# Performance work log

Hardware: AMD Instinct MI355X
Metric: run time of the kernel (lower is better)

Reference implementation:

```python
import jax, jax.numpy as jnp
import numpy as np
import math

D_MODEL = 1024
NUM_HEADS = 16
D_FF = 4096
LN_EPS = 1e-5


def _layer_norm(x, gamma, beta):
    mu = jnp.mean(x, axis=-1, keepdims=True)
    var = jnp.mean(jnp.square(x - mu), axis=-1, keepdims=True)
    return (x - mu) / jnp.sqrt(var + LN_EPS) * gamma + beta


def setup_inputs() -> dict:
    key = jax.random.key(0)
    ks = jax.random.split(key, 16)
    S, B, D, F = 2048, 2, D_MODEL, D_FF
    sc = 0.02
    inp = {
        "x": jax.random.normal(ks[0], (S, B, D), dtype=jnp.float32),
        "Wq": jax.random.normal(ks[1], (D, D), dtype=jnp.float32) * sc,
        "bq": jnp.zeros((D,), jnp.float32),
        "Wk": jax.random.normal(ks[2], (D, D), dtype=jnp.float32) * sc,
        "bk": jnp.zeros((D,), jnp.float32),
        "Wv": jax.random.normal(ks[3], (D, D), dtype=jnp.float32) * sc,
        "bv": jnp.zeros((D,), jnp.float32),
        "Wo": jax.random.normal(ks[4], (D, D), dtype=jnp.float32) * sc,
        "bo": jnp.zeros((D,), jnp.float32),
        "g1": jnp.ones((D,), jnp.float32),
        "b1": jnp.zeros((D,), jnp.float32),
        "W1": jax.random.normal(ks[5], (D, F), dtype=jnp.float32) * sc,
        "bb1": jnp.zeros((F,), jnp.float32),
        "W2": jax.random.normal(ks[6], (F, D), dtype=jnp.float32) * sc,
        "bb2": jnp.zeros((D,), jnp.float32),
        "g2": jnp.ones((D,), jnp.float32),
        "b2": jnp.zeros((D,), jnp.float32),
    }
    return inp


def reference(x, Wq, bq, Wk, bk, Wv, bv, Wo, bo, g1, b1, W1, bb1, W2, bb2, g2, b2):
    # x: [S, B, D] (seq-first, matching the torch module)
    S, B, D = x.shape
    H = NUM_HEADS
    dh = D // H

    def split_(t):  # [S, B, D] -> [B*H, S, dh]  (same as view + transpose in torch)
        return jnp.swapaxes(t.reshape(S, B * H, dh), 0, 1)

    q = split_(x @ Wq + bq)
    k = split_(x @ Wk + bk)
    v = split_(x @ Wv + bv)

    # naive bmm -> softmax -> bmm attention (full [B*H, S, S] scores)
    scores = jnp.einsum("nsd,ntd->nst", q / math.sqrt(dh), k)
    attn = jax.nn.softmax(scores, axis=-1)
    o = jnp.einsum("nst,ntd->nsd", attn, v)  # [B*H, S, dh]
    o = jnp.swapaxes(o, 0, 1).reshape(S, B, D) @ Wo + bo

    x1 = _layer_norm(x + o, g1, b1)
    ff = jax.nn.relu(x1 @ W1 + bb1) @ W2 + bb2
    return _layer_norm(x1 + ff, g2, b2)
```

## Files before the change

### kernel.cpp

```cpp
#include <hip/hip_runtime.h>
#include <hip/hip_bf16.h>
#include <cstdint>

typedef __bf16 bf16_t;
typedef __attribute__((ext_vector_type(8))) __bf16 bf16x8;
typedef __attribute__((ext_vector_type(4))) __bf16 bf16x4;
typedef __attribute__((ext_vector_type(2))) __bf16 bf16x2;
typedef __attribute__((ext_vector_type(4))) float f32x4;

#define GLOBAL_AS __attribute__((address_space(1)))
#define LDS_AS __attribute__((address_space(3)))

__device__ __forceinline__ void lds_load16(void* lds, const void* g) {
    __builtin_amdgcn_global_load_lds((GLOBAL_AS void*)g, (LDS_AS void*)lds, 16, 0, 0);
}

__global__ __launch_bounds__(256) void cast_f32_bf16(const float* __restrict__ in,
                                                     bf16_t* __restrict__ out, int n4) {
    int i = (blockIdx.x * 256 + threadIdx.x);
    if (i >= n4) return;
    float4 v = *(const float4*)(in + (size_t)i * 4);
    bf16x4 o;
    o[0] = (bf16_t)v.x; o[1] = (bf16_t)v.y; o[2] = (bf16_t)v.z; o[3] = (bf16_t)v.w;
    *(bf16x4*)(out + (size_t)i * 4) = o;
}

__global__ __launch_bounds__(256) void transpose_cast(const float* __restrict__ W,
                                                      bf16_t* __restrict__ WT,
                                                      int Kd, int Nd) {
    __shared__ float T[64][65];
    const int nbk = Kd >> 6;
    const int bk = blockIdx.x % nbk, bn = blockIdx.x / nbk;
    const int k0 = bk << 6, n0 = bn << 6;
    const int tid = threadIdx.x;
    #pragma unroll
    for (int rep = 0; rep < 4; ++rep) {
        int r = rep * 16 + (tid >> 4);
        int c = (tid & 15) * 4;
        float4 v = *(const float4*)(W + (size_t)(k0 + r) * Nd + n0 + c);
        T[r][c] = v.x; T[r][c + 1] = v.y; T[r][c + 2] = v.z; T[r][c + 3] = v.w;
    }
    __syncthreads();
    #pragma unroll
    for (int rep = 0; rep < 4; ++rep) {
        int r = rep * 16 + (tid >> 4);
        int c = (tid & 15) * 4;
        bf16x4 o;
        o[0] = (bf16_t)T[c][r]; o[1] = (bf16_t)T[c + 1][r];
        o[2] = (bf16_t)T[c + 2][r]; o[3] = (bf16_t)T[c + 3][r];
        *(bf16x4*)(WT + (size_t)(n0 + r) * Kd + k0 + c) = o;
    }
}

__global__ __launch_bounds__(256) void concat_bias(const float* a, const float* b,
                                                   const float* c, float* o) {
    int i = blockIdx.x * 256 + threadIdx.x;
    o[i] = (i < 1024) ? a[i] : (i < 2048) ? b[i - 1024] : c[i - 2048];
}

template <int OM, bool RELU>
__global__ __launch_bounds__(512, 2) void gemm256(const bf16_t* __restrict__ A,
                                                  const bf16_t* __restrict__ Bt,
                                                  const float* __restrict__ bias,
                                                  void* __restrict__ Cv,
                                                  int M, int N, int K,
                                                  int kc_len, int n_kc) {
    __shared__ alignas(16) bf16_t As[2][256 * 64];
    __shared__ alignas(16) bf16_t Bs[2][256 * 64];
    const int tid = threadIdx.x;
    const int wid = tid >> 6, lane = tid & 63;
    const int lr = lane & 15, lg = lane >> 4;
    const int wr = wid >> 2, wc = wid & 3;
    const int lrsw = (lr & 7) << 4;

    const int nbn = N >> 8;
    const int nbase = (M >> 8) * nbn;
    const int nwg = nbase * n_kc;
    int bid = blockIdx.x;
    int wg;
    if ((nwg & 7) == 0) { int q = nwg >> 3; wg = (bid & 7) * q + (bid >> 3); }
    else wg = bid;
    const int kc = wg / nbase;
    const int inner = wg - kc * nbase;
    const int bm = inner / nbn, bn = inner % nbn;

    f32x4 acc[8][4];
    #pragma unroll
    for (int i = 0; i < 8; ++i)
        #pragma unroll
        for (int j = 0; j < 4; ++j) acc[i][j] = f32x4{0.f, 0.f, 0.f, 0.f};

    const int srow = wid * 16 + (lane >> 3);
    const int colbyte = (((lane & 7) ^ (lane >> 3)) << 4);
    const char* gA = (const char*)(A + ((size_t)(bm * 256 + srow) * K + kc * kc_len)) + colbyte;
    const char* gB = (const char*)(Bt + ((size_t)(bn * 256 + srow) * K + kc * kc_len)) + colbyte;
    const size_t rs8 = (size_t)8 * K * 2;
    const size_t rs128 = (size_t)128 * K * 2;

    auto stA = [&](int b, int half, int kt) {
        char* d = (char*)As[b] + (half * 128 + wid * 16) * 128;
        const char* s = gA + (size_t)half * rs128 + (size_t)kt * 128;
        lds_load16(d, s);
        lds_load16(d + 1024, s + rs8);
    };
    auto stB = [&](int b, int half, int kt) {
        char* d = (char*)Bs[b] + (half * 128 + wid * 16) * 128;
        const char* s = gB + (size_t)half * rs128 + (size_t)kt * 128;
        lds_load16(d, s);
        lds_load16(d + 1024, s + rs8);
    };
    auto ldA = [&](int b, int m, int kk) {
        const int row = (m >> 2) * 128 + (m & 3) * 32 + wr * 16 + lr;
        return *(const bf16x8*)((const char*)As[b] + row * 128 + ((kk * 64 + lg * 16) ^ lrsw));
    };
    auto ldB = [&](int b, int n, int kk) {
        const int row = n * 64 + wc * 16 + lr;
        return *(const bf16x8*)((const char*)Bs[b] + row * 128 + ((kk * 64 + lg * 16) ^ lrsw));
    };

    const int NT = kc_len >> 6;
    stA(0, 0, 0); stB(0, 0, 0); stB(0, 1, 0); stA(0, 1, 0);
    asm volatile("s_waitcnt vmcnt(4)" ::: "memory");
    __builtin_amdgcn_s_barrier();

    bf16x8 afr[4][2], bfr[4][2];
    #pragma unroll 1
    for (int kt = 0; kt < NT; ++kt) {
        const int buf = kt & 1;
        const int ktn = (kt + 1 < NT) ? kt + 1 : kt;

        #pragma unroll
        for (int m = 0; m < 4; ++m) {
            afr[m][0] = ldA(buf, m, 0);
            afr[m][1] = ldA(buf, m, 1);
        }
        #pragma unroll
        for (int n = 0; n < 2; ++n) {
            bfr[n][0] = ldB(buf, n, 0);
            bfr[n][1] = ldB(buf, n, 1);
        }
        stA(buf ^ 1, 0, ktn);
        __builtin_amdgcn_s_barrier();
        __builtin_amdgcn_s_setprio(1);
        #pragma unroll
        for (int m = 0; m < 4; ++m)
            #pragma unroll
            for (int n = 0; n < 2; ++n) {
                acc[m][n] = __builtin_amdgcn_mfma_f32_16x16x32_bf16(afr[m][0], bfr[n][0], acc[m][n], 0, 0, 0);
                acc[m][n] = __builtin_amdgcn_mfma_f32_16x16x32_bf16(afr[m][1], bfr[n][1], acc[m][n], 0, 0, 0);
            }
        __builtin_amdgcn_s_setprio(0);
        asm volatile("s_waitcnt vmcnt(4)" ::: "memory");
        __builtin_amdgcn_s_barrier();

        #pragma unroll
        for (int n = 2; n < 4; ++n) {
            bfr[n][0] = ldB(buf, n, 0);
            bfr[n][1] = ldB(buf, n, 1);
        }
        stB(buf ^ 1, 0, ktn);
        __builtin_amdgcn_s_barrier();
        __builtin_amdgcn_s_setprio(1);
        #pragma unroll
        for (int m = 0; m < 4; ++m)
            #pragma unroll
            for (int n = 2; n < 4; ++n) {
                acc[m][n] = __builtin_amdgcn_mfma_f32_16x16x32_bf16(afr[m][0], bfr[n][0], acc[m][n], 0, 0, 0);
                acc[m][n] = __builtin_amdgcn_mfma_f32_16x16x32_bf16(afr[m][1], bfr[n][1], acc[m][n], 0, 0, 0);
            }
        __builtin_amdgcn_s_setprio(0);
        asm volatile("s_waitcnt vmcnt(4)" ::: "memory");
        __builtin_amdgcn_s_barrier();

        #pragma unroll
        for (int m = 0; m < 4; ++m) {
            afr[m][0] = ldA(buf, m + 4, 0);
            afr[m][1] = ldA(buf, m + 4, 1);
        }
        stB(buf ^ 1, 1, ktn);
        __builtin_amdgcn_s_barrier();
        __builtin_amdgcn_s_setprio(1);
        #pragma unroll
        for (int m = 0; m < 4; ++m)
            #pragma unroll
            for (int n = 0; n < 2; ++n) {
                acc[m + 4][n] = __builtin_amdgcn_mfma_f32_16x16x32_bf16(afr[m][0], bfr[n][0], acc[m + 4][n], 0, 0, 0);
                acc[m + 4][n] = __builtin_amdgcn_mfma_f32_16x16x32_bf16(afr[m][1], bfr[n][1], acc[m + 4][n], 0, 0, 0);
            }
        __builtin_amdgcn_s_setprio(0);
        __builtin_amdgcn_s_barrier();

        stA(buf ^ 1, 1, ktn);
        __builtin_amdgcn_s_barrier();
        __builtin_amdgcn_s_setprio(1);
        #pragma unroll
        for (int m = 0; m < 4; ++m)
            #pragma unroll
            for (int n = 2; n < 4; ++n) {
                acc[m + 4][n] = __builtin_amdgcn_mfma_f32_16x16x32_bf16(afr[m][0], bfr[n][0], acc[m + 4][n], 0, 0, 0);
                acc[m + 4][n] = __builtin_amdgcn_mfma_f32_16x16x32_bf16(afr[m][1], bfr[n][1], acc[m + 4][n], 0, 0, 0);
            }
        __builtin_amdgcn_s_setprio(0);
        asm volatile("s_waitcnt vmcnt(4)" ::: "memory");
        __builtin_amdgcn_s_barrier();
    }

    float* outf = (float*)Cv + (size_t)kc * M * N;
    bf16_t* outb = (bf16_t*)Cv + (size_t)kc * M * N;
    float bv[4];
    #pragma unroll
    for (int n = 0; n < 4; ++n) {
        const int c = (bn << 8) + n * 64 + wc * 16 + lr;
        bv[n] = (bias && kc == 0) ? bias[c] : 0.f;
    }
    #pragma unroll
    for (int m = 0; m < 8; ++m) {
        const int row0 = (bm << 8) + (m >> 2) * 128 + (m & 3) * 32 + wr * 16 + (lg << 2);
        #pragma unroll
        for (int n = 0; n < 4; ++n) {
            const int c = (bn << 8) + n * 64 + wc * 16 + lr;
            #pragma unroll
            for (int j = 0; j < 4; ++j) {
                float v = acc[m][n][j] + bv[n];
                if (RELU) v = fmaxf(v, 0.f);
                if (OM == 0)      ((bf16_t*)Cv)[(size_t)(row0 + j) * N + c] = (bf16_t)v;
                else if (OM == 1) outf[(size_t)(row0 + j) * N + c] = v;
                else              outb[(size_t)(row0 + j) * N + c] = (bf16_t)v;
            }
        }
    }
}

__global__ __launch_bounds__(256) void reshape_qkv(const bf16_t* __restrict__ QKV,
                                                   bf16_t* __restrict__ Q,
                                                   bf16_t* __restrict__ Kh,
                                                   bf16_t* __restrict__ VT) {
    __shared__ alignas(16) bf16_t Vl[64][72];
    const int n = blockIdx.x >> 5, st = blockIdx.x & 31;
    const int b = n >> 4, h = n & 15;
    const int s0 = st << 6;
    const int tid = threadIdx.x;
    const float qscale = 0.125f * 1.4426950408889634f;

    #pragma unroll
    for (int mat = 0; mat < 2; ++mat) {
        bf16_t* dst = mat ? Kh : Q;
        #pragma unroll
        for (int rep = 0; rep < 2; ++rep) {
            int chunk = rep * 256 + tid;
            int sl = chunk >> 3, c8 = (chunk & 7) << 3;
            size_t srow = (size_t)(s0 + sl) * 2 + b;
            bf16x8 v = *(const bf16x8*)(QKV + srow * 3072 + mat * 1024 + h * 64 + c8);
            if (mat == 0) {
                #pragma unroll
                for (int e = 0; e < 8; ++e) v[e] = (bf16_t)((float)v[e] * qscale);
            }
            *(bf16x8*)(dst + ((size_t)n * 2048 + s0 + sl) * 64 + c8) = v;
        }
    }
    #pragma unroll
    for (int rep = 0; rep < 2; ++rep) {
        int chunk = rep * 256 + tid;
        int sl = chunk >> 3, c8 = (chunk & 7) << 3;
        size_t srow = (size_t)(s0 + sl) * 2 + b;
        *(bf16x8*)&Vl[sl][c8] = *(const bf16x8*)(QKV + srow * 3072 + 2048 + h * 64 + c8);
    }
    __syncthreads();
    #pragma unroll
    for (int rep = 0; rep < 2; ++rep) {
        int chunk = rep * 256 + tid;
        int d = chunk >> 3, c8 = (chunk & 7) << 3;
        bf16x8 v;
        #pragma unroll
        for (int e = 0; e < 8; ++e) v[e] = Vl[c8 + e][d];
        *(bf16x8*)(VT + ((size_t)n * 64 + d) * 2048 + s0 + c8) = v;
    }
}

__global__ __launch_bounds__(256) void attn_fwd(const bf16_t* __restrict__ Q,
                                                const bf16_t* __restrict__ K,
                                                const bf16_t* __restrict__ VT,
                                                bf16_t* __restrict__ O) {
    const int S = 2048;
    const int n = blockIdx.x >> 4;
    const int qt = blockIdx.x & 15;
    const int q0 = qt << 7;
    const int tid = threadIdx.x, wid = tid >> 6, lane = tid & 63;
    const int lr = lane & 15, lg = lane >> 4;
    const int lrsw = (lr & 7) << 4;

    __shared__ alignas(16) bf16_t Ks[2][64 * 64];
    __shared__ alignas(16) bf16_t Vs[2][64 * 64];
    __shared__ alignas(16) bf16_t Ps[4][2][16 * 64];

    char* pbs0 = (char*)&Ps[wid][0][0];
    char* pbs1 = (char*)&Ps[wid][1][0];

    const bf16_t* Qrow0 = Q + ((size_t)n * S + q0 + wid * 32 + lr) * 64;
    const bf16_t* Qrow1 = Qrow0 + 16 * 64;
    const bf16x8 qa0 = *(const bf16x8*)(Qrow0 + lg * 8);
    const bf16x8 qa1 = *(const bf16x8*)(Qrow0 + 32 + lg * 8);
    const bf16x8 qb0 = *(const bf16x8*)(Qrow1 + lg * 8);
    const bf16x8 qb1 = *(const bf16x8*)(Qrow1 + 32 + lg * 8);

    bf16x8 ones;
    #pragma unroll
    for (int e = 0; e < 8; ++e) ones[e] = (bf16_t)1.0f;

    const int colbyte = (((lane & 7) ^ (lane >> 3)) << 4);
    const char* ksrc0 = (const char*)(K + ((size_t)n * S + wid * 16 + (lane >> 3)) * 64) + colbyte;
    const char* ksrc1 = ksrc0 + (size_t)8 * 128;
    const char* vsrc0 = (const char*)(VT + ((size_t)n * 64 + wid * 16 + (lane >> 3)) * S) + colbyte;
    const char* vsrc1 = vsrc0 + (size_t)8 * S * 2;

    auto stage = [&](int b, int t0) {
        lds_load16((char*)Ks[b] + wid * 2048,        ksrc0 + (size_t)t0 * 128);
        lds_load16((char*)Ks[b] + wid * 2048 + 1024, ksrc1 + (size_t)t0 * 128);
        lds_load16((char*)Vs[b] + wid * 2048,        vsrc0 + (size_t)t0 * 2);
        lds_load16((char*)Vs[b] + wid * 2048 + 1024, vsrc1 + (size_t)t0 * 2);
    };

    f32x4 oaccA[4], oaccB[4];
    #pragma unroll
    for (int i = 0; i < 4; ++i) {
        oaccA[i] = f32x4{0.f, 0.f, 0.f, 0.f};
        oaccB[i] = f32x4{0.f, 0.f, 0.f, 0.f};
    }
    f32x4 laccA = f32x4{0.f, 0.f, 0.f, 0.f};
    f32x4 laccB = f32x4{0.f, 0.f, 0.f, 0.f};

    stage(0, 0);
    int buf = 0;

    #pragma unroll 1
    for (int t0 = 0; t0 < S; t0 += 64) {
        if (t0 + 64 < S) {
            stage(buf ^ 1, t0 + 64);
            asm volatile("s_waitcnt vmcnt(4)" ::: "memory");
        } else {
            asm volatile("s_waitcnt vmcnt(0)" ::: "memory");
        }
        __builtin_amdgcn_s_barrier();

        const char* kb = (char*)Ks[buf];
        const char* vb = (char*)Vs[buf];

        f32x4 swA[4], swB[4];
        #pragma unroll
        for (int tc = 0; tc < 4; ++tc) {
            const char* krow = kb + (tc * 16 + lr) * 128;
            bf16x8 kf0 = *(const bf16x8*)(krow + ((lg * 16) ^ lrsw));
            bf16x8 kf1 = *(const bf16x8*)(krow + ((64 + lg * 16) ^ lrsw));
            f32x4 za = f32x4{-12.f, -12.f, -12.f, -12.f};
            za = __builtin_amdgcn_mfma_f32_16x16x32_bf16(kf0, qa0, za, 0, 0, 0);
            za = __builtin_amdgcn_mfma_f32_16x16x32_bf16(kf1, qa1, za, 0, 0, 0);
            swA[tc] = za;
            f32x4 zb = f32x4{-12.f, -12.f, -12.f, -12.f};
            zb = __builtin_amdgcn_mfma_f32_16x16x32_bf16(kf0, qb0, zb, 0, 0, 0);
            zb = __builtin_amdgcn_mfma_f32_16x16x32_bf16(kf1, qb1, zb, 0, 0, 0);
            swB[tc] = zb;
        }

        #pragma unroll
        for (int tc = 0; tc < 4; ++tc)
            #pragma unroll
            for (int j = 0; j < 4; ++j) {
                swA[tc][j] = __builtin_amdgcn_exp2f(swA[tc][j]);
                swB[tc][j] = __builtin_amdgcn_exp2f(swB[tc][j]);
            }

        #pragma unroll
        for (int tc = 0; tc < 4; ++tc)
            #pragma unroll
            for (int hh = 0; hh < 2; ++hh) {
                bf16x2 pa, pb;
                pa[0] = (bf16_t)swA[tc][2 * hh]; pa[1] = (bf16_t)swA[tc][2 * hh + 1];
                pb[0] = (bf16_t)swB[tc][2 * hh]; pb[1] = (bf16_t)swB[tc][2 * hh + 1];
                const int off = (tc * 32 + lg * 8 + hh * 4) ^ lrsw;
                *(bf16x2*)(pbs0 + lr * 128 + off) = pa;
                *(bf16x2*)(pbs1 + lr * 128 + off) = pb;
            }
        bf16x8 pA0 = *(const bf16x8*)(pbs0 + lr * 128 + ((lg * 16) ^ lrsw));
        bf16x8 pA1 = *(const bf16x8*)(pbs0 + lr * 128 + ((64 + lg * 16) ^ lrsw));
        bf16x8 pB0 = *(const bf16x8*)(pbs1 + lr * 128 + ((lg * 16) ^ lrsw));
        bf16x8 pB1 = *(const bf16x8*)(pbs1 + lr * 128 + ((64 + lg * 16) ^ lrsw));

        laccA = __builtin_amdgcn_mfma_f32_16x16x32_bf16(ones, pA0, laccA, 0, 0, 0);
        laccA = __builtin_amdgcn_mfma_f32_16x16x32_bf16(ones, pA1, laccA, 0, 0, 0);
        laccB = __builtin_amdgcn_mfma_f32_16x16x32_bf16(ones, pB0, laccB, 0, 0, 0);
        laccB = __builtin_amdgcn_mfma_f32_16x16x32_bf16(ones, pB1, laccB, 0, 0, 0);

        #pragma unroll
        for (int vc = 0; vc < 4; ++vc) {
            const char* vrow = vb + (vc * 16 + lr) * 128;
            bf16x8 vf0 = *(const bf16x8*)(vrow + ((lg * 16) ^ lrsw));
            bf16x8 vf1 = *(const bf16x8*)(vrow + ((64 + lg * 16) ^ lrsw));
            oaccA[vc] = __builtin_amdgcn_mfma_f32_16x16x32_bf16(vf0, pA0, oaccA[vc], 0, 0, 0);
            oaccA[vc] = __builtin_amdgcn_mfma_f32_16x16x32_bf16(vf1, pA1, oaccA[vc], 0, 0, 0);
            oaccB[vc] = __builtin_amdgcn_mfma_f32_16x16x32_bf16(vf0, pB0, oaccB[vc], 0, 0, 0);
            oaccB[vc] = __builtin_amdgcn_mfma_f32_16x16x32_bf16(vf1, pB1, oaccB[vc], 0, 0, 0);
        }
        __builtin_amdgcn_s_barrier();
        buf ^= 1;
    }

    const int b = n >> 4, h = n & 15;
    const float invA = 1.0f / laccA[0];
    const float invB = 1.0f / laccB[0];
    const size_t tokA = (size_t)(q0 + wid * 32 + lr) * 2 + b;
    const size_t tokB = tokA + 32;
    #pragma unroll
    for (int vc = 0; vc < 4; ++vc) {
        bf16x4 oa, ob;
        #pragma unroll
        for (int j = 0; j < 4; ++j) {
            oa[j] = (bf16_t)(oaccA[vc][j] * invA);
            ob[j] = (bf16_t)(oaccB[vc][j] * invB);
        }
        *(bf16x4*)(O + tokA * 1024 + h * 64 + vc * 16 + lg * 4) = oa;
        *(bf16x4*)(O + tokB * 1024 + h * 64 + vc * 16 + lg * 4) = ob;
    }
}

template <int P>
__global__ __launch_bounds__(256) void ln_res(const float* __restrict__ X,
                                              const bf16_t* __restrict__ Y,
                                              const float* __restrict__ g,
                                              const float* __restrict__ be,
                                              float* __restrict__ outf,
                                              bf16_t* __restrict__ outb) {
    const int row = blockIdx.x, tid = threadIdx.x;
    const size_t base = (size_t)row * 1024 + tid * 4;
    const size_t pstride = (size_t)4096 * 1024;
    float4 xv = *(const float4*)(X + base);
    float v0 = xv.x, v1 = xv.y, v2 = xv.z, v3 = xv.w;
    #pragma unroll
    for (int p = 0; p < P; ++p) {
        bf16x4 yv = *(const bf16x4*)(Y + p * pstride + base);
        v0 += (float)yv[0]; v1 += (float)yv[1]; v2 += (float)yv[2]; v3 += (float)yv[3];
    }
    float s = v0 + v1 + v2 + v3;
    float sq = v0 * v0 + v1 * v1 + v2 * v2 + v3 * v3;
    #pragma unroll
    for (int m = 1; m < 64; m <<= 1) {
        s += __shfl_xor(s, m);
        sq += __shfl_xor(sq, m);
    }
    __shared__ float rs[4], rq[4];
    const int wid = tid >> 6;
    if ((tid & 63) == 0) { rs[wid] = s; rq[wid] = sq; }
    __syncthreads();
    s = rs[0] + rs[1] + rs[2] + rs[3];
    sq = rq[0] + rq[1] + rq[2] + rq[3];
    const float mu = s * (1.f / 1024.f);
    const float var = sq * (1.f / 1024.f) - mu * mu;
    const float rstd = rsqrtf(var + 1e-5f);
    float4 gv = *(const float4*)(g + tid * 4);
    float4 bv = *(const float4*)(be + tid * 4);
    float o0 = (v0 - mu) * rstd * gv.x + bv.x;
    float o1 = (v1 - mu) * rstd * gv.y + bv.y;
    float o2 = (v2 - mu) * rstd * gv.z + bv.z;
    float o3 = (v3 - mu) * rstd * gv.w + bv.w;
    float4 ov = {o0, o1, o2, o3};
    *(float4*)(outf + base) = ov;
    if (outb) {
        bf16x4 ob;
        ob[0] = (bf16_t)o0; ob[1] = (bf16_t)o1; ob[2] = (bf16_t)o2; ob[3] = (bf16_t)o3;
        *(bf16x4*)(outb + base) = ob;
    }
}

extern "C" void kernel_launch(void* const* d_in, const int* in_sizes, int n_in,
                              void* d_out, int out_size, void* d_ws, size_t ws_size,
                              hipStream_t stream) {
    (void)in_sizes; (void)n_in; (void)out_size; (void)ws_size;
    const float* x   = (const float*)d_in[0];
    const float* Wq  = (const float*)d_in[1];
    const float* bq  = (const float*)d_in[2];
    const float* Wk  = (const float*)d_in[3];
    const float* bk  = (const float*)d_in[4];
    const float* Wv  = (const float*)d_in[5];
    const float* bv  = (const float*)d_in[6];
    const float* Wo  = (const float*)d_in[7];
    const float* bo  = (const float*)d_in[8];
    const float* g1  = (const float*)d_in[9];
    const float* b1  = (const float*)d_in[10];
    const float* W1  = (const float*)d_in[11];
    const float* bb1 = (const float*)d_in[12];
    const float* W2  = (const float*)d_in[13];
    const float* bb2 = (const float*)d_in[14];
    const float* g2  = (const float*)d_in[15];
    const float* b2  = (const float*)d_in[16];
    float* out = (float*)d_out;

    char* ws = (char*)d_ws;
    const size_t MB = 1ull << 20;
    bf16_t* xb    = (bf16_t*)(ws + 0);
    bf16_t* WqkvT = (bf16_t*)(ws + 8 * MB);
    bf16_t* WoT   = (bf16_t*)(ws + 14 * MB);
    bf16_t* W1T   = (bf16_t*)(ws + 16 * MB);
    bf16_t* W2T   = (bf16_t*)(ws + 24 * MB);
    float*  qkvb  = (float*)(ws + 32 * MB);
    bf16_t* QKV   = (bf16_t*)(ws + 33 * MB);
    bf16_t* WoP   = (bf16_t*)(ws + 33 * MB);
    bf16_t* W2P   = (bf16_t*)(ws + 33 * MB);
    bf16_t* Qh    = (bf16_t*)(ws + 65 * MB);
    bf16_t* Kh    = (bf16_t*)(ws + 73 * MB);
    bf16_t* VTh   = (bf16_t*)(ws + 81 * MB);
    float*  x1f   = (float*)(ws + 97 * MB);
    bf16_t* x1b   = (bf16_t*)(ws + 113 * MB);
    bf16_t* Hff   = (bf16_t*)(ws + 121 * MB);
    bf16_t* Otok  = (bf16_t*)(ws + 153 * MB);

    cast_f32_bf16<<<4096, 256, 0, stream>>>(x, xb, 1024 * 1024);
    transpose_cast<<<256, 256, 0, stream>>>(Wq, WqkvT, 1024, 1024);
    transpose_cast<<<256, 256, 0, stream>>>(Wk, WqkvT + 1024 * 1024, 1024, 1024);
    transpose_cast<<<256, 256, 0, stream>>>(Wv, WqkvT + 2048 * 1024, 1024, 1024);
    transpose_cast<<<256, 256, 0, stream>>>(Wo, WoT, 1024, 1024);
    transpose_cast<<<1024, 256, 0, stream>>>(W1, W1T, 1024, 4096);
    transpose_cast<<<1024, 256, 0, stream>>>(W2, W2T, 4096, 1024);
    concat_bias<<<12, 256, 0, stream>>>(bq, bk, bv, qkvb);

    gemm256<0, false><<<192, 512, 0, stream>>>(xb, WqkvT, qkvb, QKV, 4096, 3072, 1024, 1024, 1);
    reshape_qkv<<<1024, 256, 0, stream>>>(QKV, Qh, Kh, VTh);
    attn_fwd<<<512, 256, 0, stream>>>(Qh, Kh, VTh, Otok);
    gemm256<2, false><<<256, 512, 0, stream>>>(Otok, WoT, bo, WoP, 4096, 1024, 1024, 256, 4);
    ln_res<4><<<4096, 256, 0, stream>>>(x, WoP, g1, b1, x1f, x1b);

    gemm256<0, true><<<256, 512, 0, stream>>>(x1b, W1T, bb1, Hff, 4096, 4096, 1024, 1024, 1);
    gemm256<2, false><<<256, 512, 0, stream>>>(Hff, W2T, bb2, W2P, 4096, 1024, 4096, 1024, 4);
    ln_res<4><<<4096, 256, 0, stream>>>(x1f, W2P, g2, b2, out, nullptr);
}
```

Baseline: 248.1 us.

## Load V tiles directly into registers instead of staging through LDS

The attention kernel stops staging V through shared memory. Each wave now loads its V fragments straight from global memory into registers with inline-asm dwordx4 loads. The next tile's loads are double-buffered in two register arrays, with manual vmcnt waits that separate the K LDS loads from the V register loads. This removes V LDS traffic and its share of the LDS budget, at the cost of each of the four waves re-reading the same V data from global/L2 and of higher register pressure. The hand-counted vmcnt values and inline asm outputs the compiler does not know are asynchronous are a correctness and scheduling risk.

```diff
diff --git a/kernel.cpp b/kernel.cpp
--- a/kernel.cpp
+++ b/kernel.cpp
@@ -13,6 +13,12 @@
 
 __device__ __forceinline__ void lds_load16(void* lds, const void* g) {
     __builtin_amdgcn_global_load_lds((GLOBAL_AS void*)g, (LDS_AS void*)lds, 16, 0, 0);
+}
+
+__device__ __forceinline__ bf16x8 vload16(const void* p) {
+    bf16x8 r;
+    asm volatile("global_load_dwordx4 %0, %1, off" : "=&v"(r) : "v"(p));
+    return r;
 }
 
 __global__ __launch_bounds__(256) void cast_f32_bf16(const float* __restrict__ in,
@@ -290,7 +296,6 @@
     const int lrsw = (lr & 7) << 4;
 
     __shared__ alignas(16) bf16_t Ks[2][64 * 64];
-    __shared__ alignas(16) bf16_t Vs[2][64 * 64];
     __shared__ alignas(16) bf16_t Ps[4][2][16 * 64];
 
     char* pbs0 = (char*)&Ps[wid][0][0];
@@ -310,15 +315,7 @@
     const int colbyte = (((lane & 7) ^ (lane >> 3)) << 4);
     const char* ksrc0 = (const char*)(K + ((size_t)n * S + wid * 16 + (lane >> 3)) * 64) + colbyte;
     const char* ksrc1 = ksrc0 + (size_t)8 * 128;
-    const char* vsrc0 = (const char*)(VT + ((size_t)n * 64 + wid * 16 + (lane >> 3)) * S) + colbyte;
-    const char* vsrc1 = vsrc0 + (size_t)8 * S * 2;
-
-    auto stage = [&](int b, int t0) {
-        lds_load16((char*)Ks[b] + wid * 2048,        ksrc0 + (size_t)t0 * 128);
-        lds_load16((char*)Ks[b] + wid * 2048 + 1024, ksrc1 + (size_t)t0 * 128);
-        lds_load16((char*)Vs[b] + wid * 2048,        vsrc0 + (size_t)t0 * 2);
-        lds_load16((char*)Vs[b] + wid * 2048 + 1024, vsrc1 + (size_t)t0 * 2);
-    };
+    const char* vbase = (const char*)VT + ((size_t)(n * 64 + lr) * S + lg * 8) * 2;
 
     f32x4 oaccA[4], oaccB[4];
     #pragma unroll
@@ -329,22 +326,33 @@
     f32x4 laccA = f32x4{0.f, 0.f, 0.f, 0.f};
     f32x4 laccB = f32x4{0.f, 0.f, 0.f, 0.f};
 
-    stage(0, 0);
-    int buf = 0;
-
-    #pragma unroll 1
-    for (int t0 = 0; t0 < S; t0 += 64) {
-        if (t0 + 64 < S) {
-            stage(buf ^ 1, t0 + 64);
-            asm volatile("s_waitcnt vmcnt(4)" ::: "memory");
-        } else {
-            asm volatile("s_waitcnt vmcnt(0)" ::: "memory");
-        }
-        __builtin_amdgcn_s_barrier();
-
-        const char* kb = (char*)Ks[buf];
-        const char* vb = (char*)Vs[buf];
-
+    bf16x8 vA[8], vB[8];
+
+    lds_load16((char*)Ks[0] + wid * 2048,        ksrc0);
+    lds_load16((char*)Ks[0] + wid * 2048 + 1024, ksrc1);
+    #pragma unroll
+    for (int vc = 0; vc < 4; ++vc) {
+        const char* p = vbase + (size_t)vc * (16 * 2048 * 2);
+        vA[2 * vc]     = vload16(p);
+        vA[2 * vc + 1] = vload16(p + 64);
+    }
+    asm volatile("s_waitcnt vmcnt(0)" ::: "memory");
+    __builtin_amdgcn_s_barrier();
+
+    auto tile = [&](int bufK, bf16x8 (&vcur)[8], bf16x8 (&vnext)[8], int t0) {
+        const int t0n = (t0 + 64 < S) ? t0 + 64 : t0;
+        lds_load16((char*)Ks[bufK ^ 1] + wid * 2048,        ksrc0 + (size_t)t0n * 128);
+        lds_load16((char*)Ks[bufK ^ 1] + wid * 2048 + 1024, ksrc1 + (size_t)t0n * 128);
+        #pragma unroll
+        for (int vc = 0; vc < 4; ++vc) {
+            const char* p = vbase + (size_t)vc * (16 * 2048 * 2) + (size_t)t0n * 2;
+            vnext[2 * vc]     = vload16(p);
+            vnext[2 * vc + 1] = vload16(p + 64);
+        }
+        asm volatile("s_waitcnt vmcnt(18)" ::: "memory");
+        __builtin_amdgcn_s_barrier();
+
+        const char* kb = (const char*)Ks[bufK];
         f32x4 swA[4], swB[4];
         #pragma unroll
         for (int tc = 0; tc < 4; ++tc) {
@@ -390,19 +398,23 @@
         laccB = __builtin_amdgcn_mfma_f32_16x16x32_bf16(ones, pB0, laccB, 0, 0, 0);
         laccB = __builtin_amdgcn_mfma_f32_16x16x32_bf16(ones, pB1, laccB, 0, 0, 0);
 
+        asm volatile("s_waitcnt vmcnt(10)" ::: "memory");
         #pragma unroll
         for (int vc = 0; vc < 4; ++vc) {
-            const char* vrow = vb + (vc * 16 + lr) * 128;
-            bf16x8 vf0 = *(const bf16x8*)(vrow + ((lg * 16) ^ lrsw));
-            bf16x8 vf1 = *(const bf16x8*)(vrow + ((64 + lg * 16) ^ lrsw));
-            oaccA[vc] = __builtin_amdgcn_mfma_f32_16x16x32_bf16(vf0, pA0, oaccA[vc], 0, 0, 0);
-            oaccA[vc] = __builtin_amdgcn_mfma_f32_16x16x32_bf16(vf1, pA1, oaccA[vc], 0, 0, 0);
-            oaccB[vc] = __builtin_amdgcn_mfma_f32_16x16x32_bf16(vf0, pB0, oaccB[vc], 0, 0, 0);
-            oaccB[vc] = __builtin_amdgcn_mfma_f32_16x16x32_bf16(vf1, pB1, oaccB[vc], 0, 0, 0);
-        }
-        __builtin_amdgcn_s_barrier();
-        buf ^= 1;
-    }
+            oaccA[vc] = __builtin_amdgcn_mfma_f32_16x16x32_bf16(vcur[2 * vc],     pA0, oaccA[vc], 0, 0, 0);
+            oaccA[vc] = __builtin_amdgcn_mfma_f32_16x16x32_bf16(vcur[2 * vc + 1], pA1, oaccA[vc], 0, 0, 0);
+            oaccB[vc] = __builtin_amdgcn_mfma_f32_16x16x32_bf16(vcur[2 * vc],     pB0, oaccB[vc], 0, 0, 0);
+            oaccB[vc] = __builtin_amdgcn_mfma_f32_16x16x32_bf16(vcur[2 * vc + 1], pB1, oaccB[vc], 0, 0, 0);
+        }
+        __builtin_amdgcn_s_barrier();
+    };
+
+    #pragma unroll 1
+    for (int i = 0; i < 32; i += 2) {
+        tile(0, vA, vB, i * 64);
+        tile(1, vB, vA, i * 64 + 64);
+    }
+    asm volatile("s_waitcnt vmcnt(0)" ::: "memory");
 
     const int b = n >> 4, h = n & 15;
     const float invA = 1.0f / laccA[0];
```

Result: slower. 265.6 us (+7.1%).

## Merge prep kernels into one launch and read Q/K directly from QKV

Applied to the files above, without the earlier changes.

Fuses the x cast, six weight transpose-casts and bias concat into a single prep_all launch, cutting seven kernel launches. The reshape kernel now only transposes V, and attention reads Q (scaled on load) and K directly from the token-major QKV buffer, avoiding writing and re-reading separate head-major Q/K copies. K tile loads now use a larger row stride, which may reduce load coalescing in attention. Workspace buffers are relaid out to match.

```diff
diff --git a/kernel.cpp b/kernel.cpp
--- a/kernel.cpp
+++ b/kernel.cpp
@@ -15,47 +15,65 @@
     __builtin_amdgcn_global_load_lds((GLOBAL_AS void*)g, (LDS_AS void*)lds, 16, 0, 0);
 }
 
-__global__ __launch_bounds__(256) void cast_f32_bf16(const float* __restrict__ in,
-                                                     bf16_t* __restrict__ out, int n4) {
-    int i = (blockIdx.x * 256 + threadIdx.x);
-    if (i >= n4) return;
-    float4 v = *(const float4*)(in + (size_t)i * 4);
-    bf16x4 o;
-    o[0] = (bf16_t)v.x; o[1] = (bf16_t)v.y; o[2] = (bf16_t)v.z; o[3] = (bf16_t)v.w;
-    *(bf16x4*)(out + (size_t)i * 4) = o;
-}
-
-__global__ __launch_bounds__(256) void transpose_cast(const float* __restrict__ W,
-                                                      bf16_t* __restrict__ WT,
-                                                      int Kd, int Nd) {
+__global__ __launch_bounds__(256) void prep_all(const float* __restrict__ x,
+                                                const float* __restrict__ Wq,
+                                                const float* __restrict__ Wk,
+                                                const float* __restrict__ Wv,
+                                                const float* __restrict__ Wo,
+                                                const float* __restrict__ W1,
+                                                const float* __restrict__ W2,
+                                                const float* __restrict__ bq,
+                                                const float* __restrict__ bk,
+                                                const float* __restrict__ bv,
+                                                bf16_t* __restrict__ xb,
+                                                bf16_t* __restrict__ WqkvT,
+                                                bf16_t* __restrict__ WoT,
+                                                bf16_t* __restrict__ W1T,
+                                                bf16_t* __restrict__ W2T,
+                                                float* __restrict__ qkvb) {
     __shared__ float T[64][65];
-    const int nbk = Kd >> 6;
-    const int bk = blockIdx.x % nbk, bn = blockIdx.x / nbk;
-    const int k0 = bk << 6, n0 = bn << 6;
-    const int tid = threadIdx.x;
-    #pragma unroll
-    for (int rep = 0; rep < 4; ++rep) {
-        int r = rep * 16 + (tid >> 4);
-        int c = (tid & 15) * 4;
-        float4 v = *(const float4*)(W + (size_t)(k0 + r) * Nd + n0 + c);
-        T[r][c] = v.x; T[r][c + 1] = v.y; T[r][c + 2] = v.z; T[r][c + 3] = v.w;
-    }
-    __syncthreads();
-    #pragma unroll
-    for (int rep = 0; rep < 4; ++rep) {
-        int r = rep * 16 + (tid >> 4);
-        int c = (tid & 15) * 4;
+    const int bid = blockIdx.x, tid = threadIdx.x;
+    if (bid < 3072) {
+        const float* W; bf16_t* WT; int Kd, Nd, lb;
+        if (bid < 1024) {
+            Kd = 1024; Nd = 1024; lb = bid & 255;
+            const int w = bid >> 8;
+            W  = (w == 0) ? Wq : (w == 1) ? Wk : (w == 2) ? Wv : Wo;
+            WT = (w == 0) ? WqkvT : (w == 1) ? WqkvT + 1048576
+               : (w == 2) ? WqkvT + 2097152 : WoT;
+        } else if (bid < 2048) { W = W1; WT = W1T; Kd = 1024; Nd = 4096; lb = bid - 1024; }
+        else                   { W = W2; WT = W2T; Kd = 4096; Nd = 1024; lb = bid - 2048; }
+        const int nbk = Kd >> 6;
+        const int bk = lb % nbk, bn = lb / nbk;
+        const int k0 = bk << 6, n0 = bn << 6;
+        #pragma unroll
+        for (int rep = 0; rep < 4; ++rep) {
+            int r = rep * 16 + (tid >> 4);
+            int c = (tid & 15) * 4;
+            float4 v = *(const float4*)(W + (size_t)(k0 + r) * Nd + n0 + c);
+            T[r][c] = v.x; T[r][c + 1] = v.y; T[r][c + 2] = v.z; T[r][c + 3] = v.w;
+        }
+        __syncthreads();
+        #pragma unroll
+        for (int rep = 0; rep < 4; ++rep) {
+            int r = rep * 16 + (tid >> 4);
+            int c = (tid & 15) * 4;
+            bf16x4 o;
+            o[0] = (bf16_t)T[c][r]; o[1] = (bf16_t)T[c + 1][r];
+            o[2] = (bf16_t)T[c + 2][r]; o[3] = (bf16_t)T[c + 3][r];
+            *(bf16x4*)(WT + (size_t)(n0 + r) * Kd + k0 + c) = o;
+        }
+    } else if (bid < 7168) {
+        const int i = (bid - 3072) * 256 + tid;
+        float4 v = *(const float4*)(x + (size_t)i * 4);
         bf16x4 o;
-        o[0] = (bf16_t)T[c][r]; o[1] = (bf16_t)T[c + 1][r];
-        o[2] = (bf16_t)T[c + 2][r]; o[3] = (bf16_t)T[c + 3][r];
-        *(bf16x4*)(WT + (size_t)(n0 + r) * Kd + k0 + c) = o;
-    }
-}
-
-__global__ __launch_bounds__(256) void concat_bias(const float* a, const float* b,
-                                                   const float* c, float* o) {
-    int i = blockIdx.x * 256 + threadIdx.x;
-    o[i] = (i < 1024) ? a[i] : (i < 2048) ? b[i - 1024] : c[i - 2048];
+        o[0] = (bf16_t)v.x; o[1] = (bf16_t)v.y; o[2] = (bf16_t)v.z; o[3] = (bf16_t)v.w;
+        *(bf16x4*)(xb + (size_t)i * 4) = o;
+    } else {
+        const int i = (bid - 7168) * 256 + tid;
+        if (i < 3072)
+            qkvb[i] = (i < 1024) ? bq[i] : (i < 2048) ? bk[i - 1024] : bv[i - 2048];
+    }
 }
 
 template <int OM, bool RELU>
@@ -231,33 +249,14 @@
     }
 }
 
-__global__ __launch_bounds__(256) void reshape_qkv(const bf16_t* __restrict__ QKV,
-                                                   bf16_t* __restrict__ Q,
-                                                   bf16_t* __restrict__ Kh,
-                                                   bf16_t* __restrict__ VT) {
+__global__ __launch_bounds__(256) void reshape_v(const bf16_t* __restrict__ QKV,
+                                                 bf16_t* __restrict__ VT) {
     __shared__ alignas(16) bf16_t Vl[64][72];
     const int n = blockIdx.x >> 5, st = blockIdx.x & 31;
     const int b = n >> 4, h = n & 15;
     const int s0 = st << 6;
     const int tid = threadIdx.x;
-    const float qscale = 0.125f * 1.4426950408889634f;
-
-    #pragma unroll
-    for (int mat = 0; mat < 2; ++mat) {
-        bf16_t* dst = mat ? Kh : Q;
-        #pragma unroll
-        for (int rep = 0; rep < 2; ++rep) {
-            int chunk = rep * 256 + tid;
-            int sl = chunk >> 3, c8 = (chunk & 7) << 3;
-            size_t srow = (size_t)(s0 + sl) * 2 + b;
-            bf16x8 v = *(const bf16x8*)(QKV + srow * 3072 + mat * 1024 + h * 64 + c8);
-            if (mat == 0) {
-                #pragma unroll
-                for (int e = 0; e < 8; ++e) v[e] = (bf16_t)((float)v[e] * qscale);
-            }
-            *(bf16x8*)(dst + ((size_t)n * 2048 + s0 + sl) * 64 + c8) = v;
-        }
-    }
+
     #pragma unroll
     for (int rep = 0; rep < 2; ++rep) {
         int chunk = rep * 256 + tid;
@@ -277,14 +276,14 @@
     }
 }
 
-__global__ __launch_bounds__(256) void attn_fwd(const bf16_t* __restrict__ Q,
-                                                const bf16_t* __restrict__ K,
+__global__ __launch_bounds__(256) void attn_fwd(const bf16_t* __restrict__ QKV,
                                                 const bf16_t* __restrict__ VT,
                                                 bf16_t* __restrict__ O) {
     const int S = 2048;
     const int n = blockIdx.x >> 4;
     const int qt = blockIdx.x & 15;
     const int q0 = qt << 7;
+    const int b = n >> 4, h = n & 15;
     const int tid = threadIdx.x, wid = tid >> 6, lane = tid & 63;
     const int lr = lane & 15, lg = lane >> 4;
     const int lrsw = (lr & 7) << 4;
@@ -296,28 +295,37 @@
     char* pbs0 = (char*)&Ps[wid][0][0];
     char* pbs1 = (char*)&Ps[wid][1][0];
 
-    const bf16_t* Qrow0 = Q + ((size_t)n * S + q0 + wid * 32 + lr) * 64;
-    const bf16_t* Qrow1 = Qrow0 + 16 * 64;
-    const bf16x8 qa0 = *(const bf16x8*)(Qrow0 + lg * 8);
-    const bf16x8 qa1 = *(const bf16x8*)(Qrow0 + 32 + lg * 8);
-    const bf16x8 qb0 = *(const bf16x8*)(Qrow1 + lg * 8);
-    const bf16x8 qb1 = *(const bf16x8*)(Qrow1 + 32 + lg * 8);
+    const float qsc = 0.125f * 1.4426950408889634f;
+    auto scale8 = [&](bf16x8 v) {
+        bf16x8 r;
+        #pragma unroll
+        for (int e = 0; e < 8; ++e) r[e] = (bf16_t)((float)v[e] * qsc);
+        return r;
+    };
+    const bf16_t* Qrow0 = QKV + ((size_t)(q0 + wid * 32 + lr) * 2 + b) * 3072 + h * 64;
+    const bf16_t* Qrow1 = Qrow0 + (size_t)16 * 2 * 3072;
+    const bf16x8 qa0 = scale8(*(const bf16x8*)(Qrow0 + lg * 8));
+    const bf16x8 qa1 = scale8(*(const bf16x8*)(Qrow0 + 32 + lg * 8));
+    const bf16x8 qb0 = scale8(*(const bf16x8*)(Qrow1 + lg * 8));
+    const bf16x8 qb1 = scale8(*(const bf16x8*)(Qrow1 + 32 + lg * 8));
 
     bf16x8 ones;
     #pragma unroll
     for (int e = 0; e < 8; ++e) ones[e] = (bf16_t)1.0f;
 
     const int colbyte = (((lane & 7) ^ (lane >> 3)) << 4);
-    const char* ksrc0 = (const char*)(K + ((size_t)n * S + wid * 16 + (lane >> 3)) * 64) + colbyte;
-    const char* ksrc1 = ksrc0 + (size_t)8 * 128;
+    const size_t kstride = (size_t)2 * 3072 * 2;
+    const char* ksrc0 = (const char*)QKV +
+        (((size_t)(wid * 16 + (lane >> 3)) * 2 + b) * 3072 + 1024 + h * 64) * 2 + colbyte;
+    const char* ksrc1 = ksrc0 + 8 * kstride;
     const char* vsrc0 = (const char*)(VT + ((size_t)n * 64 + wid * 16 + (lane >> 3)) * S) + colbyte;
     const char* vsrc1 = vsrc0 + (size_t)8 * S * 2;
 
-    auto stage = [&](int b, int t0) {
-        lds_load16((char*)Ks[b] + wid * 2048,        ksrc0 + (size_t)t0 * 128);
-        lds_load16((char*)Ks[b] + wid * 2048 + 1024, ksrc1 + (size_t)t0 * 128);
-        lds_load16((char*)Vs[b] + wid * 2048,        vsrc0 + (size_t)t0 * 2);
-        lds_load16((char*)Vs[b] + wid * 2048 + 1024, vsrc1 + (size_t)t0 * 2);
+    auto stage = [&](int bf, int t0) {
+        lds_load16((char*)Ks[bf] + wid * 2048,        ksrc0 + (size_t)t0 * kstride);
+        lds_load16((char*)Ks[bf] + wid * 2048 + 1024, ksrc1 + (size_t)t0 * kstride);
+        lds_load16((char*)Vs[bf] + wid * 2048,        vsrc0 + (size_t)t0 * 2);
+        lds_load16((char*)Vs[bf] + wid * 2048 + 1024, vsrc1 + (size_t)t0 * 2);
     };
 
     f32x4 oaccA[4], oaccB[4];
@@ -404,7 +412,6 @@
         buf ^= 1;
     }
 
-    const int b = n >> 4, h = n & 15;
     const float invA = 1.0f / laccA[0];
     const float invB = 1.0f / laccB[0];
     const size_t tokA = (size_t)(q0 + wid * 32 + lr) * 2 + b;
@@ -502,28 +509,20 @@
     bf16_t* W2T   = (bf16_t*)(ws + 24 * MB);
     float*  qkvb  = (float*)(ws + 32 * MB);
     bf16_t* QKV   = (bf16_t*)(ws + 33 * MB);
-    bf16_t* WoP   = (bf16_t*)(ws + 33 * MB);
+    bf16_t* VTh   = (bf16_t*)(ws + 57 * MB);
+    bf16_t* Otok  = (bf16_t*)(ws + 65 * MB);
+    bf16_t* WoP   = (bf16_t*)(ws + 73 * MB);
+    float*  x1f   = (float*)(ws + 105 * MB);
+    bf16_t* x1b   = (bf16_t*)(ws + 121 * MB);
+    bf16_t* Hff   = (bf16_t*)(ws + 129 * MB);
     bf16_t* W2P   = (bf16_t*)(ws + 33 * MB);
-    bf16_t* Qh    = (bf16_t*)(ws + 65 * MB);
-    bf16_t* Kh    = (bf16_t*)(ws + 73 * MB);
-    bf16_t* VTh   = (bf16_t*)(ws + 81 * MB);
-    float*  x1f   = (float*)(ws + 97 * MB);
-    bf16_t* x1b   = (bf16_t*)(ws + 113 * MB);
-    bf16_t* Hff   = (bf16_t*)(ws + 121 * MB);
-    bf16_t* Otok  = (bf16_t*)(ws + 153 * MB);
-
-    cast_f32_bf16<<<4096, 256, 0, stream>>>(x, xb, 1024 * 1024);
-    transpose_cast<<<256, 256, 0, stream>>>(Wq, WqkvT, 1024, 1024);
-    transpose_cast<<<256, 256, 0, stream>>>(Wk, WqkvT + 1024 * 1024, 1024, 1024);
-    transpose_cast<<<256, 256, 0, stream>>>(Wv, WqkvT + 2048 * 1024, 1024, 1024);
-    transpose_cast<<<256, 256, 0, stream>>>(Wo, WoT, 1024, 1024);
-    transpose_cast<<<1024, 256, 0, stream>>>(W1, W1T, 1024, 4096);
-    transpose_cast<<<1024, 256, 0, stream>>>(W2, W2T, 4096, 1024);
-    concat_bias<<<12, 256, 0, stream>>>(bq, bk, bv, qkvb);
+
+    prep_all<<<7180, 256, 0, stream>>>(x, Wq, Wk, Wv, Wo, W1, W2, bq, bk, bv,
+                                       xb, WqkvT, WoT, W1T, W2T, qkvb);
 
     gemm256<0, false><<<192, 512, 0, stream>>>(xb, WqkvT, qkvb, QKV, 4096, 3072, 1024, 1024, 1);
-    reshape_qkv<<<1024, 256, 0, stream>>>(QKV, Qh, Kh, VTh);
-    attn_fwd<<<512, 256, 0, stream>>>(Qh, Kh, VTh, Otok);
+    reshape_v<<<1024, 256, 0, stream>>>(QKV, VTh);
+    attn_fwd<<<512, 256, 0, stream>>>(QKV, VTh, Otok);
     gemm256<2, false><<<256, 512, 0, stream>>>(Otok, WoT, bo, WoP, 4096, 1024, 1024, 256, 4);
     ln_res<4><<<4096, 256, 0, stream>>>(x, WoP, g1, b1, x1f, x1b);
 
```

Result: faster. 230.6 us (-7.1%).
